# Kernel tuning notes

Hardware: AMD Instinct MI355X
Metric: run time of the kernel (lower is better)

## Reference

```python
import jax, jax.numpy as jnp
import numpy as np

EPS = 1e-12
BETA = 0.25

def normalise(x, axis=-1):
    return x * jax.lax.rsqrt(jnp.mean(x * x, axis=axis, keepdims=True) + EPS)

def setup_inputs() -> dict:
    key = jax.random.key(0)
    ks = jax.random.split(key, 4)
    N, F, D, C = 8192, 512, 64, 8192
    return {
        "z": jax.random.normal(ks[0], (N, F), dtype=jnp.float32),
        "W_in": jax.random.normal(ks[1], (F, D), dtype=jnp.float32) * (1.0 / np.sqrt(F)),
        "b_in": jnp.zeros((D,), dtype=jnp.float32),
        "codebook": jax.random.normal(ks[2], (C, D), dtype=jnp.float32),
        "W_out": jax.random.normal(ks[3], (D, F), dtype=jnp.float32) * (1.0 / np.sqrt(D)),
        "b_out": jnp.zeros((F,), dtype=jnp.float32),
    }

def reference(z, W_in, b_in, codebook, W_out, b_out):
    sg = jax.lax.stop_gradient
    # input projection: [N, F] -> [N, D]
    zp = z @ W_in + b_in
    zn = normalise(zp)                  # [N, D]
    cn = normalise(codebook)            # [C, D]
    # squared euclidean distance via matmul expansion (same math as
    # sum((z[:,None]-c[None])**2, -1), avoids [N,C,D] materialization)
    z_sq = jnp.sum(zn * zn, axis=-1, keepdims=True)          # [N, 1]
    c_sq = jnp.sum(cn * cn, axis=-1)[None, :]                # [1, C]
    distance = z_sq + c_sq - 2.0 * (zn @ cn.T)               # [N, C]
    idxes = jnp.argmin(distance, axis=-1)                    # [N]
    codes = normalise(codebook[idxes], axis=-1)               # [N, D]
    loss = BETA * jnp.mean((sg(zn) - codes) ** 2) + jnp.mean((zn - sg(codes)) ** 2)
    codes = zn + sg(codes - zn)                               # straight-through
    out = codes @ W_out + b_out                               # [N, F]
    return (out, loss, idxes)
```

## Files before the change

kernel.cpp:

```cpp
#include <hip/hip_runtime.h>
#include <hip/hip_bf16.h>

#define N_ROWS 8192
#define F_DIM  512
#define D_DIM  64
#define C_CODES 8192

typedef __attribute__((ext_vector_type(8))) short bf16x8;
typedef __attribute__((ext_vector_type(4))) float f32x4;

__device__ __forceinline__ unsigned short rne_bf16(float x) {
  unsigned u = __float_as_uint(x);
  return (unsigned short)((u + 0x7FFFu + ((u >> 16) & 1u)) >> 16);
}
__device__ __forceinline__ float bf16_to_f(unsigned short u) {
  return __uint_as_float(((unsigned)u) << 16);
}
__device__ __forceinline__ void limb3(const float* xs, bf16x8& H, bf16x8& M, bf16x8& L) {
  #pragma unroll
  for (int j = 0; j < 8; ++j) {
    float x = xs[j];
    unsigned short h = rne_bf16(x);
    float r1 = x - bf16_to_f(h);
    unsigned short m = rne_bf16(r1);
    float r2 = r1 - bf16_to_f(m);
    unsigned short lo = rne_bf16(r2);
    H[j] = (short)h; M[j] = (short)m; L[j] = (short)lo;
  }
}

typedef __attribute__((address_space(1))) const unsigned char gas_uchar;
typedef __attribute__((address_space(3))) unsigned char las_uchar;
__device__ __forceinline__ void gld_lds16(const void* g, void* l) {
  __builtin_amdgcn_global_load_lds((gas_uchar*)g, (las_uchar*)l, 16, 0, 0);
}

__global__ __launch_bounds__(256) void k_prep(
    const float* __restrict__ W_in, const float* __restrict__ W_out,
    const float* __restrict__ cb,
    unsigned short* __restrict__ win_sw, unsigned short* __restrict__ wout_sw,
    float* __restrict__ cn, unsigned short* __restrict__ cn_sw) {
  const int tid = threadIdx.x, w = tid >> 6, l = tid & 63;
  const int lo = l & 15, hi = l >> 4;
  const int bid = blockIdx.x;

  if (bid < 16) {
    const int task = bid * 4 + w;
    const int kc = task >> 2, cg = task & 3;
    float xs[8];
    #pragma unroll
    for (int j = 0; j < 8; ++j)
      xs[j] = W_in[(size_t)(kc * 32 + hi * 8 + j) * D_DIM + cg * 16 + lo];
    bf16x8 H, M, L;
    limb3(xs, H, M, L);
    const int fb = (kc * 4 + cg) * 3;
    unsigned short* d0 = win_sw + (size_t)(fb + 0) * 512 + l * 8;
    unsigned short* d1 = win_sw + (size_t)(fb + 1) * 512 + l * 8;
    unsigned short* d2 = win_sw + (size_t)(fb + 2) * 512 + l * 8;
    #pragma unroll
    for (int j = 0; j < 8; ++j) { d0[j] = (unsigned short)H[j]; d1[j] = (unsigned short)M[j]; d2[j] = (unsigned short)L[j]; }
  } else if (bid < 32) {
    const int task = (bid - 16) * 4 + w;
    const int cg = task >> 1, c = task & 1;
    float xs[8];
    #pragma unroll
    for (int j = 0; j < 8; ++j)
      xs[j] = W_out[(size_t)(c * 32 + hi * 8 + j) * F_DIM + cg * 16 + lo];
    bf16x8 H, M, L;
    limb3(xs, H, M, L);
    const int fb = (cg * 2 + c) * 3;
    unsigned short* d0 = wout_sw + (size_t)(fb + 0) * 512 + l * 8;
    unsigned short* d1 = wout_sw + (size_t)(fb + 1) * 512 + l * 8;
    unsigned short* d2 = wout_sw + (size_t)(fb + 2) * 512 + l * 8;
    #pragma unroll
    for (int j = 0; j < 8; ++j) { d0[j] = (unsigned short)H[j]; d1[j] = (unsigned short)M[j]; d2[j] = (unsigned short)L[j]; }
  } else {
    const int g = (bid - 32) * 4 + w;
    const int code = g * 16 + lo;
    float xs[2][8];
    float s = 0.0f;
    #pragma unroll
    for (int c = 0; c < 2; ++c) {
      const float* sp = cb + (size_t)code * D_DIM + c * 32 + hi * 8;
      float4 a = *(const float4*)sp, b = *(const float4*)(sp + 4);
      xs[c][0]=a.x; xs[c][1]=a.y; xs[c][2]=a.z; xs[c][3]=a.w;
      xs[c][4]=b.x; xs[c][5]=b.y; xs[c][6]=b.z; xs[c][7]=b.w;
      #pragma unroll
      for (int j = 0; j < 8; ++j) s += xs[c][j] * xs[c][j];
    }
    s += __shfl_xor(s, 16);
    s += __shfl_xor(s, 32);
    float inv = rsqrtf(s * (1.0f / 64.0f) + 1e-12f);
    #pragma unroll
    for (int c = 0; c < 2; ++c) {
      #pragma unroll
      for (int j = 0; j < 8; ++j) xs[c][j] *= inv;
      float* dp = cn + (size_t)code * D_DIM + c * 32 + hi * 8;
      *(float4*)dp = make_float4(xs[c][0], xs[c][1], xs[c][2], xs[c][3]);
      *(float4*)(dp + 4) = make_float4(xs[c][4], xs[c][5], xs[c][6], xs[c][7]);
      bf16x8 H, M, L;
      limb3(xs[c], H, M, L);
      const int fb = (g * 2 + c) * 3;
      unsigned short* d0 = cn_sw + (size_t)(fb + 0) * 512 + l * 8;
      unsigned short* d1 = cn_sw + (size_t)(fb + 1) * 512 + l * 8;
      unsigned short* d2 = cn_sw + (size_t)(fb + 2) * 512 + l * 8;
      #pragma unroll
      for (int j = 0; j < 8; ++j) { d0[j] = (unsigned short)H[j]; d1[j] = (unsigned short)M[j]; d2[j] = (unsigned short)L[j]; }
    }
  }
}

__global__ __launch_bounds__(256) void k_zn(
    const float* __restrict__ z, const unsigned short* __restrict__ w_in_sw,
    const float* __restrict__ b_in, float* __restrict__ zn,
    unsigned short* __restrict__ zn_sw) {
  __shared__ float red[4096];
  __shared__ float t_lds[16 * 65];
  const int tid = threadIdx.x, w = tid >> 6, l = tid & 63;
  const int lo = l & 15, hi = l >> 4;
  const int g = blockIdx.x;
  const int r0 = g * 16;
  const int kcb = w * 4;
  const bf16x8* Bptr = (const bf16x8*)w_in_sw;
  const float* zbase = z + (size_t)(r0 + lo) * F_DIM + hi * 8;

  f32x4 acc[4];
  #pragma unroll
  for (int cg = 0; cg < 4; ++cg) acc[cg] = (f32x4){0.f, 0.f, 0.f, 0.f};

  bf16x8 Bu[12], Bv[12];
  #pragma unroll
  for (int i = 0; i < 12; ++i) Bu[i] = Bptr[((size_t)kcb * 12 + i) * 64 + l];
  float4 za = *(const float4*)(zbase + kcb * 32);
  float4 zb = *(const float4*)(zbase + kcb * 32 + 4);

  #define ZMFMA(BCUR)                                                         \
    {                                                                         \
      float xs[8] = {za.x, za.y, za.z, za.w, zb.x, zb.y, zb.z, zb.w};         \
      bf16x8 Ah, Am, Al;                                                      \
      limb3(xs, Ah, Am, Al);                                                  \
      _Pragma("unroll")                                                       \
      for (int cg = 0; cg < 4; ++cg) {                                        \
        f32x4 t = acc[cg];                                                    \
        t = __builtin_amdgcn_mfma_f32_16x16x32_bf16(Ah, BCUR[cg*3+0], t, 0,0,0); \
        t = __builtin_amdgcn_mfma_f32_16x16x32_bf16(Ah, BCUR[cg*3+1], t, 0,0,0); \
        t = __builtin_amdgcn_mfma_f32_16x16x32_bf16(Am, BCUR[cg*3+0], t, 0,0,0); \
        t = __builtin_amdgcn_mfma_f32_16x16x32_bf16(Ah, BCUR[cg*3+2], t, 0,0,0); \
        t = __builtin_amdgcn_mfma_f32_16x16x32_bf16(Al, BCUR[cg*3+0], t, 0,0,0); \
        t = __builtin_amdgcn_mfma_f32_16x16x32_bf16(Am, BCUR[cg*3+1], t, 0,0,0); \
        acc[cg] = t;                                                          \
      }                                                                       \
    }

  {
    float4 na = *(const float4*)(zbase + (kcb + 1) * 32);
    float4 nb = *(const float4*)(zbase + (kcb + 1) * 32 + 4);
    #pragma unroll
    for (int i = 0; i < 12; ++i) Bv[i] = Bptr[((size_t)(kcb + 1) * 12 + i) * 64 + l];
    ZMFMA(Bu)
    za = na; zb = nb;
  }
  {
    float4 na = *(const float4*)(zbase + (kcb + 2) * 32);
    float4 nb = *(const float4*)(zbase + (kcb + 2) * 32 + 4);
    #pragma unroll
    for (int i = 0; i < 12; ++i) Bu[i] = Bptr[((size_t)(kcb + 2) * 12 + i) * 64 + l];
    ZMFMA(Bv)
    za = na; zb = nb;
  }
  {
    float4 na = *(const float4*)(zbase + (kcb + 3) * 32);
    float4 nb = *(const float4*)(zbase + (kcb + 3) * 32 + 4);
    #pragma unroll
    for (int i = 0; i < 12; ++i) Bv[i] = Bptr[((size_t)(kcb + 3) * 12 + i) * 64 + l];
    ZMFMA(Bu)
    za = na; zb = nb;
  }
  ZMFMA(Bv)
  #undef ZMFMA

  #pragma unroll
  for (int cg = 0; cg < 4; ++cg)
    #pragma unroll
    for (int r = 0; r < 4; ++r)
      red[((w * 4 + cg) * 4 + r) * 64 + l] = acc[cg][r];
  __syncthreads();

  {
    float v[4], s = 0.0f;
    #pragma unroll
    for (int cg = 0; cg < 4; ++cg) {
      float t = b_in[cg * 16 + lo];
      #pragma unroll
      for (int w2 = 0; w2 < 4; ++w2) t += red[((w2 * 4 + cg) * 4 + w) * 64 + l];
      v[cg] = t; s += t * t;
    }
    s += __shfl_xor(s, 1);
    s += __shfl_xor(s, 2);
    s += __shfl_xor(s, 4);
    s += __shfl_xor(s, 8);
    float inv = rsqrtf(s * (1.0f / 64.0f) + 1e-12f);
    #pragma unroll
    for (int cg = 0; cg < 4; ++cg)
      t_lds[(hi * 4 + w) * 65 + cg * 16 + lo] = v[cg] * inv;
  }
  __syncthreads();

  if (w < 2) {
    const int c = w;
    float xs[8];
    #pragma unroll
    for (int j = 0; j < 8; ++j) xs[j] = t_lds[lo * 65 + c * 32 + hi * 8 + j];
    float* dp = zn + (size_t)(r0 + lo) * D_DIM + c * 32 + hi * 8;
    *(float4*)dp = make_float4(xs[0], xs[1], xs[2], xs[3]);
    *(float4*)(dp + 4) = make_float4(xs[4], xs[5], xs[6], xs[7]);
    bf16x8 H, M, L;
    limb3(xs, H, M, L);
    const int fb = (g * 2 + c) * 3;
    unsigned short* d0 = zn_sw + (size_t)(fb + 0) * 512 + l * 8;
    unsigned short* d1 = zn_sw + (size_t)(fb + 1) * 512 + l * 8;
    unsigned short* d2 = zn_sw + (size_t)(fb + 2) * 512 + l * 8;
    #pragma unroll
    for (int j = 0; j < 8; ++j) { d0[j] = (unsigned short)H[j]; d1[j] = (unsigned short)M[j]; d2[j] = (unsigned short)L[j]; }
  }
}

__global__ __launch_bounds__(256) void k_argmax(
    const unsigned short* __restrict__ zn_sw,
    const unsigned short* __restrict__ cn_sw,
    float* __restrict__ pval, int* __restrict__ pidx) {
  __shared__ short smem[2 * 12 * 512];
  const int tid = threadIdx.x;
  const int w = tid >> 6, l = tid & 63;
  const int lo = l & 15, hi = l >> 4;
  const int gA0 = (blockIdx.x * 4 + w) * 2;
  const int gB0 = blockIdx.y * 32;
  const bf16x8* Ab = (const bf16x8*)zn_sw;
  const char* Bbytes = (const char*)cn_sw;

  bf16x8 A0[2][3], A1[2][3];
  #pragma unroll
  for (int c = 0; c < 2; ++c)
    #pragma unroll
    for (int m = 0; m < 3; ++m) {
      A0[c][m] = Ab[(size_t)((gA0 * 2 + c) * 3 + m) * 64 + l];
      A1[c][m] = Ab[(size_t)(((gA0 + 1) * 2 + c) * 3 + m) * 64 + l];
    }

  float bv[8];
  int bi[8];
  #pragma unroll
  for (int i = 0; i < 8; ++i) { bv[i] = -1e30f; bi[i] = 0; }
  int cand = blockIdx.y * 512 + lo;

  #define STAGE(b, s)                                                         \
    {                                                                         \
      const int fb = (gB0 + (s) * 2) * 6 + w * 3;                             \
      _Pragma("unroll")                                                       \
      for (int i = 0; i < 3; ++i)                                             \
        gld_lds16(Bbytes + ((size_t)(fb + i) << 10) + (size_t)l * 16,         \
                  &smem[((b) * 12 + w * 3 + i) * 512]);                       \
    }

  #define MF(A_, B_, C_) __builtin_amdgcn_mfma_f32_16x16x32_bf16(A_, B_, C_, 0, 0, 0)

  #define COMPUTE(LF)                                                         \
    {                                                                         \
      bf16x8 Bf[6];                                                           \
      _Pragma("unroll")                                                       \
      for (int i = 0; i < 6; ++i)                                             \
        Bf[i] = *(const bf16x8*)&smem[((LF) + i) * 512 + l * 8];              \
      f32x4 a0 = {0.f,0.f,0.f,0.f}, a1 = {0.f,0.f,0.f,0.f};                   \
      f32x4 a2 = {0.f,0.f,0.f,0.f}, a3 = {0.f,0.f,0.f,0.f};                   \
      a0 = MF(A0[0][0], Bf[0], a0); a1 = MF(A0[1][0], Bf[3], a1);             \
      a2 = MF(A1[0][0], Bf[0], a2); a3 = MF(A1[1][0], Bf[3], a3);             \
      a0 = MF(A0[0][0], Bf[1], a0); a1 = MF(A0[1][0], Bf[4], a1);             \
      a2 = MF(A1[0][0], Bf[1], a2); a3 = MF(A1[1][0], Bf[4], a3);             \
      a0 = MF(A0[0][1], Bf[0], a0); a1 = MF(A0[1][1], Bf[3], a1);             \
      a2 = MF(A1[0][1], Bf[0], a2); a3 = MF(A1[1][1], Bf[3], a3);             \
      a0 = MF(A0[0][0], Bf[2], a0); a1 = MF(A0[1][0], Bf[5], a1);             \
      a2 = MF(A1[0][0], Bf[2], a2); a3 = MF(A1[1][0], Bf[5], a3);             \
      a0 = MF(A0[0][2], Bf[0], a0); a1 = MF(A0[1][2], Bf[3], a1);             \
      a2 = MF(A1[0][2], Bf[0], a2); a3 = MF(A1[1][2], Bf[3], a3);             \
      a0 = MF(A0[0][1], Bf[1], a0); a1 = MF(A0[1][1], Bf[4], a1);             \
      a2 = MF(A1[0][1], Bf[1], a2); a3 = MF(A1[1][1], Bf[4], a3);             \
      _Pragma("unroll")                                                       \
      for (int r = 0; r < 4; ++r) {                                           \
        float d0 = a0[r] + a1[r];                                             \
        if (d0 > bv[r]) { bv[r] = d0; bi[r] = cand; }                         \
        float d1 = a2[r] + a3[r];                                             \
        if (d1 > bv[4 + r]) { bv[4 + r] = d1; bi[4 + r] = cand; }             \
      }                                                                       \
      cand += 16;                                                             \
    }

  STAGE(0, 0)
  __syncthreads();
  int cur = 0;
  for (int s = 0; s < 16; ++s) {
    if (s < 15) STAGE(cur ^ 1, s + 1)
    COMPUTE(cur * 12 + 0)
    COMPUTE(cur * 12 + 6)
    __syncthreads();
    cur ^= 1;
  }
  #undef STAGE
  #undef COMPUTE
  #undef MF

  #pragma unroll
  for (int i = 0; i < 8; ++i) {
    float v = bv[i]; int ix = bi[i];
    #pragma unroll
    for (int m = 1; m < 16; m <<= 1) {
      float ov = __shfl_xor(v, m);
      int oi = __shfl_xor(ix, m);
      if (ov > v || (ov == v && oi < ix)) { v = ov; ix = oi; }
    }
    bv[i] = v; bi[i] = ix;
  }
  if (lo == 0) {
    int off = blockIdx.y * N_ROWS;
    int base0 = gA0 * 16 + hi * 4;
    int base1 = (gA0 + 1) * 16 + hi * 4;
    #pragma unroll
    for (int r = 0; r < 4; ++r) {
      pval[off + base0 + r] = bv[r];     pidx[off + base0 + r] = bi[r];
      pval[off + base1 + r] = bv[4 + r]; pidx[off + base1 + r] = bi[4 + r];
    }
  }
}

__global__ __launch_bounds__(256) void k_out(
    const float* __restrict__ cn, const float* __restrict__ zn,
    const float* __restrict__ pval, const int* __restrict__ pidx,
    const unsigned short* __restrict__ w_out_sw,
    const float* __restrict__ b_out, float* __restrict__ out,
    float* __restrict__ idx_f, float* __restrict__ pl) {
  const int tid = threadIdx.x, w = tid >> 6, l = tid & 63;
  const int lo = l & 15, hi = l >> 4;
  const int r0 = blockIdx.x * 16;
  const int row = r0 + lo;

  float v = pval[row];
  int ix = pidx[row];
  #pragma unroll
  for (int q = 1; q < 16; ++q) {
    float vq = pval[q * N_ROWS + row];
    int iq = pidx[q * N_ROWS + row];
    if (vq > v) { v = vq; ix = iq; }
  }
  if (w == 0 && hi == 0) idx_f[row] = (float)ix;

  bf16x8 A[2][3];
  float lp = 0.0f;
  #pragma unroll
  for (int c = 0; c < 2; ++c) {
    const float* cp = cn + (size_t)ix * D_DIM + c * 32 + hi * 8;
    const float* zp = zn + (size_t)row * D_DIM + c * 32 + hi * 8;
    float4 c0 = *(const float4*)cp, c1 = *(const float4*)(cp + 4);
    float4 z0 = *(const float4*)zp, z1 = *(const float4*)(zp + 4);
    float xs[8] = {c0.x, c0.y, c0.z, c0.w, c1.x, c1.y, c1.z, c1.w};
    float zs[8] = {z0.x, z0.y, z0.z, z0.w, z1.x, z1.y, z1.z, z1.w};
    limb3(xs, A[c][0], A[c][1], A[c][2]);
    #pragma unroll
    for (int j = 0; j < 8; ++j) { float d = xs[j] - zs[j]; lp += d * d; }
  }
  if (w == 0) {
    #pragma unroll
    for (int m = 1; m < 64; m <<= 1) lp += __shfl_xor(lp, m);
    if (l == 0) pl[blockIdx.x] = lp;
  }

  const bf16x8* Bptr = (const bf16x8*)w_out_sw;
  const int cgb = w * 8;
  bf16x8 Bu[6], Bv[6];
  #pragma unroll
  for (int i = 0; i < 6; ++i) Bu[i] = Bptr[((size_t)cgb * 6 + i) * 64 + l];

  #define OSTEP(BCUR, BNXT, CG)                                               \
    {                                                                         \
      _Pragma("unroll")                                                       \
      for (int i = 0; i < 6; ++i)                                             \
        BNXT[i] = Bptr[((size_t)((CG) + 1) * 6 + i) * 64 + l];                \
      f32x4 a0 = {0.f,0.f,0.f,0.f}, a1 = {0.f,0.f,0.f,0.f};                   \
      a0 = __builtin_amdgcn_mfma_f32_16x16x32_bf16(A[0][0], BCUR[0], a0, 0,0,0); \
      a1 = __builtin_amdgcn_mfma_f32_16x16x32_bf16(A[1][0], BCUR[3], a1, 0,0,0); \
      a0 = __builtin_amdgcn_mfma_f32_16x16x32_bf16(A[0][0], BCUR[1], a0, 0,0,0); \
      a1 = __builtin_amdgcn_mfma_f32_16x16x32_bf16(A[1][0], BCUR[4], a1, 0,0,0); \
      a0 = __builtin_amdgcn_mfma_f32_16x16x32_bf16(A[0][1], BCUR[0], a0, 0,0,0); \
      a1 = __builtin_amdgcn_mfma_f32_16x16x32_bf16(A[1][1], BCUR[3], a1, 0,0,0); \
      a0 = __builtin_amdgcn_mfma_f32_16x16x32_bf16(A[0][0], BCUR[2], a0, 0,0,0); \
      a1 = __builtin_amdgcn_mfma_f32_16x16x32_bf16(A[1][0], BCUR[5], a1, 0,0,0); \
      a0 = __builtin_amdgcn_mfma_f32_16x16x32_bf16(A[0][2], BCUR[0], a0, 0,0,0); \
      a1 = __builtin_amdgcn_mfma_f32_16x16x32_bf16(A[1][2], BCUR[3], a1, 0,0,0); \
      a0 = __builtin_amdgcn_mfma_f32_16x16x32_bf16(A[0][1], BCUR[1], a0, 0,0,0); \
      a1 = __builtin_amdgcn_mfma_f32_16x16x32_bf16(A[1][1], BCUR[4], a1, 0,0,0); \
      float bb = b_out[(CG) * 16 + lo];                                       \
      _Pragma("unroll")                                                       \
      for (int r = 0; r < 4; ++r)                                             \
        out[(size_t)(r0 + hi * 4 + r) * F_DIM + (CG) * 16 + lo] =             \
            a0[r] + a1[r] + bb;                                               \
    }

  for (int cg = cgb; cg < cgb + 8; cg += 2) {
    OSTEP(Bu, Bv, cg)
    OSTEP(Bv, Bu, cg + 1)
  }
  #undef OSTEP
}

__global__ __launch_bounds__(64) void k_loss_final(
    const float* __restrict__ pl, float* __restrict__ loss_out) {
  const int l = threadIdx.x;
  float s = 0.0f;
  #pragma unroll
  for (int i = 0; i < 8; ++i) s += pl[l + 64 * i];
  #pragma unroll
  for (int m = 1; m < 64; m <<= 1) s += __shfl_xor(s, m);
  if (l == 0) loss_out[0] = s * (1.25f / (float)(N_ROWS * D_DIM));
}

extern "C" void kernel_launch(void* const* d_in, const int* in_sizes, int n_in,
                              void* d_out, int out_size, void* d_ws, size_t ws_size,
                              hipStream_t stream) {
  const float* z        = (const float*)d_in[0];
  const float* W_in     = (const float*)d_in[1];
  const float* b_in     = (const float*)d_in[2];
  const float* codebook = (const float*)d_in[3];
  const float* W_out    = (const float*)d_in[4];
  const float* b_out    = (const float*)d_in[5];

  float* outp   = (float*)d_out;
  float* loss_f = outp + (size_t)N_ROWS * F_DIM;
  float* idx_f  = loss_f + 1;

  float* wsf = (float*)d_ws;
  float* zn_ws = wsf;
  float* cn_ws = wsf + 524288;
  unsigned short* zn_sw = (unsigned short*)(wsf + 1048576);
  unsigned short* cn_sw = (unsigned short*)(wsf + 1835008);
  unsigned short* win_sw  = (unsigned short*)(wsf + 2625536);
  unsigned short* wout_sw = (unsigned short*)(wsf + 2674688);
  float* pval_ws = wsf + 2723840;
  int*   pidx_ws = (int*)(wsf + 2854912);
  float* pl_ws   = wsf + 2985984;

  hipLaunchKernelGGL(k_prep, dim3(160), dim3(256), 0, stream,
                     W_in, W_out, codebook, win_sw, wout_sw, cn_ws, cn_sw);
  hipLaunchKernelGGL(k_zn, dim3(512), dim3(256), 0, stream,
                     z, win_sw, b_in, zn_ws, zn_sw);
  hipLaunchKernelGGL(k_argmax, dim3(64, 16), dim3(256), 0, stream,
                     zn_sw, cn_sw, pval_ws, pidx_ws);
  hipLaunchKernelGGL(k_out, dim3(512), dim3(256), 0, stream,
                     cn_ws, zn_ws, pval_ws, pidx_ws, wout_sw, b_out,
                     outp, idx_f, pl_ws);
  hipLaunchKernelGGL(k_loss_final, dim3(1), dim3(64), 0, stream,
                     pl_ws, loss_f);
}
```

Baseline: 141.6 us.

## Stage z through swizzled LDS, vectorize limb stores, split k_out grid, atomic loss

```diff
diff --git a/kernel.cpp b/kernel.cpp
--- a/kernel.cpp
+++ b/kernel.cpp
@@ -39,10 +39,12 @@
     const float* __restrict__ W_in, const float* __restrict__ W_out,
     const float* __restrict__ cb,
     unsigned short* __restrict__ win_sw, unsigned short* __restrict__ wout_sw,
-    float* __restrict__ cn, unsigned short* __restrict__ cn_sw) {
+    float* __restrict__ cn, unsigned short* __restrict__ cn_sw,
+    float* __restrict__ loss_f) {
   const int tid = threadIdx.x, w = tid >> 6, l = tid & 63;
   const int lo = l & 15, hi = l >> 4;
   const int bid = blockIdx.x;
+  if (bid == 0 && tid == 0) loss_f[0] = 0.0f;
 
   if (bid < 16) {
     const int task = bid * 4 + w;
@@ -55,10 +57,9 @@
     limb3(xs, H, M, L);
     const int fb = (kc * 4 + cg) * 3;
     unsigned short* d0 = win_sw + (size_t)(fb + 0) * 512 + l * 8;
-    unsigned short* d1 = win_sw + (size_t)(fb + 1) * 512 + l * 8;
-    unsigned short* d2 = win_sw + (size_t)(fb + 2) * 512 + l * 8;
-    #pragma unroll
-    for (int j = 0; j < 8; ++j) { d0[j] = (unsigned short)H[j]; d1[j] = (unsigned short)M[j]; d2[j] = (unsigned short)L[j]; }
+    *(bf16x8*)d0 = H;
+    *(bf16x8*)(d0 + 512) = M;
+    *(bf16x8*)(d0 + 1024) = L;
   } else if (bid < 32) {
     const int task = (bid - 16) * 4 + w;
     const int cg = task >> 1, c = task & 1;
@@ -70,10 +71,9 @@
     limb3(xs, H, M, L);
     const int fb = (cg * 2 + c) * 3;
     unsigned short* d0 = wout_sw + (size_t)(fb + 0) * 512 + l * 8;
-    unsigned short* d1 = wout_sw + (size_t)(fb + 1) * 512 + l * 8;
-    unsigned short* d2 = wout_sw + (size_t)(fb + 2) * 512 + l * 8;
-    #pragma unroll
-    for (int j = 0; j < 8; ++j) { d0[j] = (unsigned short)H[j]; d1[j] = (unsigned short)M[j]; d2[j] = (unsigned short)L[j]; }
+    *(bf16x8*)d0 = H;
+    *(bf16x8*)(d0 + 512) = M;
+    *(bf16x8*)(d0 + 1024) = L;
   } else {
     const int g = (bid - 32) * 4 + w;
     const int code = g * 16 + lo;
@@ -102,10 +102,9 @@
       limb3(xs[c], H, M, L);
       const int fb = (g * 2 + c) * 3;
       unsigned short* d0 = cn_sw + (size_t)(fb + 0) * 512 + l * 8;
-      unsigned short* d1 = cn_sw + (size_t)(fb + 1) * 512 + l * 8;
-      unsigned short* d2 = cn_sw + (size_t)(fb + 2) * 512 + l * 8;
-      #pragma unroll
-      for (int j = 0; j < 8; ++j) { d0[j] = (unsigned short)H[j]; d1[j] = (unsigned short)M[j]; d2[j] = (unsigned short)L[j]; }
+      *(bf16x8*)d0 = H;
+      *(bf16x8*)(d0 + 512) = M;
+      *(bf16x8*)(d0 + 1024) = L;
     }
   }
 }
@@ -114,15 +113,24 @@
     const float* __restrict__ z, const unsigned short* __restrict__ w_in_sw,
     const float* __restrict__ b_in, float* __restrict__ zn,
     unsigned short* __restrict__ zn_sw) {
-  __shared__ float red[4096];
-  __shared__ float t_lds[16 * 65];
+  __shared__ __attribute__((aligned(16))) float zlds[8192];
+  float* red = zlds;
+  float* t_lds = zlds + 4096;
   const int tid = threadIdx.x, w = tid >> 6, l = tid & 63;
   const int lo = l & 15, hi = l >> 4;
   const int g = blockIdx.x;
   const int r0 = g * 16;
   const int kcb = w * 4;
   const bf16x8* Bptr = (const bf16x8*)w_in_sw;
-  const float* zbase = z + (size_t)(r0 + lo) * F_DIM + hi * 8;
+  const char* zB = (const char*)(z + (size_t)r0 * F_DIM);
+  char* zbytes = (char*)zlds;
+
+  #pragma unroll
+  for (int i = 0; i < 8; ++i) {
+    const int p = (w * 8 + i) * 1024 + l * 16;
+    const int r = p >> 11, o = p & 2047;
+    gld_lds16(zB + (size_t)r * 2048 + (o ^ ((r & 7) << 4)), zbytes + p);
+  }
 
   f32x4 acc[4];
   #pragma unroll
@@ -131,11 +139,22 @@
   bf16x8 Bu[12], Bv[12];
   #pragma unroll
   for (int i = 0; i < 12; ++i) Bu[i] = Bptr[((size_t)kcb * 12 + i) * 64 + l];
-  float4 za = *(const float4*)(zbase + kcb * 32);
-  float4 zb = *(const float4*)(zbase + kcb * 32 + 4);
-
-  #define ZMFMA(BCUR)                                                         \
+
+  __syncthreads();
+
+  const int swz = (lo & 7) << 4;
+  const int rowb = lo * 2048;
+
+  #define ZSTEP(BCUR, BNXT, KC, PREF)                                         \
     {                                                                         \
+      if (PREF) {                                                             \
+        _Pragma("unroll")                                                     \
+        for (int i = 0; i < 12; ++i)                                          \
+          BNXT[i] = Bptr[((size_t)((KC) + 1) * 12 + i) * 64 + l];             \
+      }                                                                       \
+      const int C = (KC) * 128 + hi * 32;                                     \
+      float4 za = *(const float4*)(zbytes + rowb + ((C) ^ swz));              \
+      float4 zb = *(const float4*)(zbytes + rowb + (((C) + 16) ^ swz));       \
       float xs[8] = {za.x, za.y, za.z, za.w, zb.x, zb.y, zb.z, zb.w};         \
       bf16x8 Ah, Am, Al;                                                      \
       limb3(xs, Ah, Am, Al);                                                  \
@@ -152,32 +171,13 @@
       }                                                                       \
     }
 
-  {
-    float4 na = *(const float4*)(zbase + (kcb + 1) * 32);
-    float4 nb = *(const float4*)(zbase + (kcb + 1) * 32 + 4);
-    #pragma unroll
-    for (int i = 0; i < 12; ++i) Bv[i] = Bptr[((size_t)(kcb + 1) * 12 + i) * 64 + l];
-    ZMFMA(Bu)
-    za = na; zb = nb;
-  }
-  {
-    float4 na = *(const float4*)(zbase + (kcb + 2) * 32);
-    float4 nb = *(const float4*)(zbase + (kcb + 2) * 32 + 4);
-    #pragma unroll
-    for (int i = 0; i < 12; ++i) Bu[i] = Bptr[((size_t)(kcb + 2) * 12 + i) * 64 + l];
-    ZMFMA(Bv)
-    za = na; zb = nb;
-  }
-  {
-    float4 na = *(const float4*)(zbase + (kcb + 3) * 32);
-    float4 nb = *(const float4*)(zbase + (kcb + 3) * 32 + 4);
-    #pragma unroll
-    for (int i = 0; i < 12; ++i) Bv[i] = Bptr[((size_t)(kcb + 3) * 12 + i) * 64 + l];
-    ZMFMA(Bu)
-    za = na; zb = nb;
-  }
-  ZMFMA(Bv)
-  #undef ZMFMA
+  ZSTEP(Bu, Bv, kcb + 0, 1)
+  ZSTEP(Bv, Bu, kcb + 1, 1)
+  ZSTEP(Bu, Bv, kcb + 2, 1)
+  ZSTEP(Bv, Bu, kcb + 3, 0)
+  #undef ZSTEP
+
+  __syncthreads();
 
   #pragma unroll
   for (int cg = 0; cg < 4; ++cg)
@@ -218,10 +218,9 @@
     limb3(xs, H, M, L);
     const int fb = (g * 2 + c) * 3;
     unsigned short* d0 = zn_sw + (size_t)(fb + 0) * 512 + l * 8;
-    unsigned short* d1 = zn_sw + (size_t)(fb + 1) * 512 + l * 8;
-    unsigned short* d2 = zn_sw + (size_t)(fb + 2) * 512 + l * 8;
-    #pragma unroll
-    for (int j = 0; j < 8; ++j) { d0[j] = (unsigned short)H[j]; d1[j] = (unsigned short)M[j]; d2[j] = (unsigned short)L[j]; }
+    *(bf16x8*)d0 = H;
+    *(bf16x8*)(d0 + 512) = M;
+    *(bf16x8*)(d0 + 1024) = L;
   }
 }
 
@@ -336,7 +335,7 @@
     const float* __restrict__ pval, const int* __restrict__ pidx,
     const unsigned short* __restrict__ w_out_sw,
     const float* __restrict__ b_out, float* __restrict__ out,
-    float* __restrict__ idx_f, float* __restrict__ pl) {
+    float* __restrict__ idx_f, float* __restrict__ loss_f) {
   const int tid = threadIdx.x, w = tid >> 6, l = tid & 63;
   const int lo = l & 15, hi = l >> 4;
   const int r0 = blockIdx.x * 16;
@@ -350,7 +349,7 @@
     int iq = pidx[q * N_ROWS + row];
     if (vq > v) { v = vq; ix = iq; }
   }
-  if (w == 0 && hi == 0) idx_f[row] = (float)ix;
+  if (blockIdx.y == 0 && w == 0 && hi == 0) idx_f[row] = (float)ix;
 
   bf16x8 A[2][3];
   float lp = 0.0f;
@@ -366,14 +365,14 @@
     #pragma unroll
     for (int j = 0; j < 8; ++j) { float d = xs[j] - zs[j]; lp += d * d; }
   }
-  if (w == 0) {
+  if (blockIdx.y == 0 && w == 0) {
     #pragma unroll
     for (int m = 1; m < 64; m <<= 1) lp += __shfl_xor(lp, m);
-    if (l == 0) pl[blockIdx.x] = lp;
+    if (l == 0) atomicAdd(loss_f, lp * (1.25f / (float)(N_ROWS * D_DIM)));
   }
 
   const bf16x8* Bptr = (const bf16x8*)w_out_sw;
-  const int cgb = w * 8;
+  const int cgb = blockIdx.y * 16 + w * 4;
   bf16x8 Bu[6], Bv[6];
   #pragma unroll
   for (int i = 0; i < 6; ++i) Bu[i] = Bptr[((size_t)cgb * 6 + i) * 64 + l];
@@ -403,22 +402,11 @@
             a0[r] + a1[r] + bb;                                               \
     }
 
-  for (int cg = cgb; cg < cgb + 8; cg += 2) {
+  for (int cg = cgb; cg < cgb + 4; cg += 2) {
     OSTEP(Bu, Bv, cg)
     OSTEP(Bv, Bu, cg + 1)
   }
   #undef OSTEP
-}
-
-__global__ __launch_bounds__(64) void k_loss_final(
-    const float* __restrict__ pl, float* __restrict__ loss_out) {
-  const int l = threadIdx.x;
-  float s = 0.0f;
-  #pragma unroll
-  for (int i = 0; i < 8; ++i) s += pl[l + 64 * i];
-  #pragma unroll
-  for (int m = 1; m < 64; m <<= 1) s += __shfl_xor(s, m);
-  if (l == 0) loss_out[0] = s * (1.25f / (float)(N_ROWS * D_DIM));
 }
 
 extern "C" void kernel_launch(void* const* d_in, const int* in_sizes, int n_in,
@@ -444,17 +432,15 @@
   unsigned short* wout_sw = (unsigned short*)(wsf + 2674688);
   float* pval_ws = wsf + 2723840;
   int*   pidx_ws = (int*)(wsf + 2854912);
-  float* pl_ws   = wsf + 2985984;
 
   hipLaunchKernelGGL(k_prep, dim3(160), dim3(256), 0, stream,
-                     W_in, W_out, codebook, win_sw, wout_sw, cn_ws, cn_sw);
+                     W_in, W_out, codebook, win_sw, wout_sw, cn_ws, cn_sw,
+                     loss_f);
   hipLaunchKernelGGL(k_zn, dim3(512), dim3(256), 0, stream,
                      z, win_sw, b_in, zn_ws, zn_sw);
   hipLaunchKernelGGL(k_argmax, dim3(64, 16), dim3(256), 0, stream,
                      zn_sw, cn_sw, pval_ws, pidx_ws);
-  hipLaunchKernelGGL(k_out, dim3(512), dim3(256), 0, stream,
+  hipLaunchKernelGGL(k_out, dim3(512, 2), dim3(256), 0, stream,
                      cn_ws, zn_ws, pval_ws, pidx_ws, wout_sw, b_out,
-                     outp, idx_f, pl_ws);
-  hipLaunchKernelGGL(k_loss_final, dim3(1), dim3(64), 0, stream,
-                     pl_ws, loss_f);
-}
+                     outp, idx_f, loss_f);
+}
```

Measured after the change: 149.4 us. +5.5%, slower.
